# Kernel optimization log

Hardware: AMD Instinct MI355X
Metric: run time of the kernel (lower is better)

Reference implementation:

```python
import jax, jax.numpy as jnp
import numpy as np

# Per-task block sizes, sorted descending (powers of 2), as in _InverseLogDetCache
N = (262144, 65536, 16384)
TOTAL = 262144 + 65536 + 16384  # 344064
DIAG_SHIFT = 10.0  # keeps Schur complement S away from 0 (plays role of noise)


def setup_inputs() -> dict:
    key = jax.random.key(0)
    ks = jax.random.split(key, 14)
    rn = lambda k, n: jax.random.normal(k, (n,), dtype=jnp.float32)
    return {
        "lam00_re": rn(ks[0], N[0]) + DIAG_SHIFT,
        "lam00_im": rn(ks[1], N[0]),
        "lam01_re": rn(ks[2], N[0]),
        "lam01_im": rn(ks[3], N[0]),
        "lam02_re": rn(ks[4], N[0]),
        "lam02_im": rn(ks[5], N[0]),
        "lam11_re": rn(ks[6], N[1]) + DIAG_SHIFT,
        "lam11_im": rn(ks[7], N[1]),
        "lam12_re": rn(ks[8], N[1]),
        "lam12_im": rn(ks[9], N[1]),
        "lam22_re": rn(ks[10], N[2]) + DIAG_SHIFT,
        "lam22_im": rn(ks[11], N[2]),
        "z_re": rn(ks[12], TOTAL),
        "z_im": rn(ks[13], TOTAL),
    }


def _step(A, B, lam_ll, n_l):
    """One recursive block Schur-complement update.
    A: (Ra, Ra, na) complex current inverse; B: (Ra*r, n_l) off-diag lam block;
    lam_ll: (n_l,) diagonal lam; returns updated A (R+1, R+1, n_l) and logdet inc."""
    Ra, na = A.shape[0], A.shape[-1]
    r = na // n_l
    Bvec = B.reshape(Ra, -1)                              # (Ra, na)
    T = (Bvec[None, :, :] * A).sum(1).reshape(-1, n_l)    # (R, n_l), R = Ra*r
    M = (B.conj() * T).sum(0)                             # (n_l,)
    S = lam_ll - M                                        # Schur complement diag
    logdet_inc = jnp.log(jnp.abs(S)).sum()
    P = T / S                                             # (R, n_l)
    C = P[:, None, :] * T[None, :, :].conj()              # (R, R, n_l)
    # scatter-add old inverse A into the refined block structure of C
    ii0, ii1, ii2 = jnp.meshgrid(jnp.arange(Ra), jnp.arange(Ra), jnp.arange(na), indexing='ij')
    ii0, ii1, ii2 = ii0.ravel(), ii1.ravel(), ii2.ravel()
    jj0 = ii2 % n_l
    jj1 = ii2 // n_l
    C = C.at[ii0 * r + jj1, ii1 * r + jj1, jj0].add(A.reshape(-1))
    ur = jnp.concatenate([C, -P[:, None, :]], axis=1)                       # (R, R+1, n_l)
    br = jnp.concatenate([-P.conj()[None, :, :], (1.0 / S)[None, None, :]], axis=1)  # (1, R+1, n_l)
    return jnp.concatenate([ur, br], axis=0), logdet_inc


def _forward(lams, z):
    A = (1.0 / lams[(0, 0)])[None, None, :]               # (1, 1, N[0])
    logdet = jnp.log(jnp.abs(lams[(0, 0)])).sum()
    for l in range(1, len(N)):
        B = jnp.concatenate([lams[(k, l)] for k in range(l)], axis=0).reshape(-1, N[l])
        A, inc = _step(A, B, lams[(l, l)], N[l])
        logdet = logdet + inc
    # tilde-to-tilde gram matrix solve: z (TOTAL,) -> (1, R, n_min) * A, sum block rows
    n_min = N[-1]
    zb = z.reshape(1, -1, n_min)                          # (1, 21, n_min)
    zout = (zb * A).sum(-2).reshape(-1)                   # (TOTAL,)
    return A, logdet, zout


def reference(lam00_re, lam00_im, lam01_re, lam01_im, lam02_re, lam02_im,
              lam11_re, lam11_im, lam12_re, lam12_im, lam22_re, lam22_im,
              z_re, z_im):
    lams = {
        (0, 0): lam00_re + 1j * lam00_im,
        (0, 1): lam01_re + 1j * lam01_im,
        (0, 2): lam02_re + 1j * lam02_im,
        (1, 1): lam11_re + 1j * lam11_im,
        (1, 2): lam12_re + 1j * lam12_im,
        (2, 2): lam22_re + 1j * lam22_im,
    }
    z = z_re + 1j * z_im
    A, logdet, zout = _forward(lams, z)
    return (jnp.stack([A.real, A.imag]), logdet, jnp.stack([zout.real, zout.imag]))
```

## Files before the change

kernel.cpp:

```cpp
#include <hip/hip_runtime.h>

#define N2 16384
#define N1 65536

#define OUT_AIM 7225344
#define OUT_LD  14450688
#define OUT_ZRE 14450689
#define OUT_ZIM 14794753

#define L_T2R  0
#define L_T2I  1280
#define L_M2   2560
#define L_SC   3072
#define L_IS2R 9728
#define L_IS2I 9792
#define L_RED  9856
#define L_TOT  9864

#define SC(idx, u, jl) lds[L_SC + (((idx)*4 + (u)) * 64) + (jl)]

#define NTST2(addr, v0, v1) do {                                   \
    union { float f[2]; long L; } _u; _u.f[0] = (v0); _u.f[1] = (v1); \
    __builtin_nontemporal_store(_u.L, (long*)(addr)); } while (0)

__global__ __launch_bounds__(448) void fused_kernel(
    const float* __restrict__ l00r, const float* __restrict__ l00i,
    const float* __restrict__ l01r, const float* __restrict__ l01i,
    const float* __restrict__ l02r, const float* __restrict__ l02i,
    const float* __restrict__ l11r, const float* __restrict__ l11i,
    const float* __restrict__ l12r, const float* __restrict__ l12i,
    const float* __restrict__ l22r, const float* __restrict__ l22i,
    const float* __restrict__ zre,  const float* __restrict__ zim,
    float* __restrict__ out, double* __restrict__ ld_partial)
{
    __shared__ float lds[L_TOT];
    const int t   = threadIdx.x;
    const int jl  = t & 63;
    const int j0  = blockIdx.x * 64;
    const bool y0 = (blockIdx.y == 0);
    float ld = 0.f;

    if (t < 256) {
        const int u = t >> 6;
        const int m = u * N2 + (j0 + jl);

        float i0r[4], i0i[4], t1r[4], t1i[4], p1r[4], p1i[4];
        float m1r = 0.f, m1i = 0.f;
#pragma unroll
        for (int k = 0; k < 4; ++k) {
            const int i = k * N1 + m;
            const float ar = l00r[i], ai = l00i[i];
            const float br = l01r[i], bi = l01i[i];
            const float d  = ar*ar + ai*ai;
            const float rd = 1.f / d;
            if (y0) ld += 0.5f * logf(d);
            const float xr = ar * rd, xi = -ai * rd;
            i0r[k] = xr; i0i[k] = xi;
            const float tr = br*xr - bi*xi;
            const float ti = br*xi + bi*xr;
            t1r[k] = tr; t1i[k] = ti;
            m1r += br*tr + bi*ti;
            m1i += br*ti - bi*tr;
        }
        const float s1r = l11r[m] - m1r;
        const float s1i = l11i[m] - m1i;
        const float ds1 = s1r*s1r + s1i*s1i;
        if (y0) ld += 0.5f * logf(ds1);
        const float rds1 = 1.f / ds1;
        const float is1r = s1r * rds1, is1i = -s1i * rds1;
#pragma unroll
        for (int k = 0; k < 4; ++k) {
            p1r[k] = t1r[k]*is1r - t1i[k]*is1i;
            p1i[k] = t1r[k]*is1i + t1i[k]*is1r;
        }

        float bcr[5], bci[5];
#pragma unroll
        for (int a = 0; a < 4; ++a) { bcr[a] = l02r[a*N1+m]; bci[a] = l02i[a*N1+m]; }
        bcr[4] = l12r[m]; bci[4] = l12i[m];

        float wr = -bcr[4], wi = -bci[4];
#pragma unroll
        for (int b = 0; b < 4; ++b) {
            wr += bcr[b]*t1r[b] + bci[b]*t1i[b];
            wi += bci[b]*t1r[b] - bcr[b]*t1i[b];
        }
        float ur[5], ui[5];
#pragma unroll
        for (int a = 0; a < 4; ++a) {
            ur[a] = p1r[a]*wr - p1i[a]*wi + bcr[a]*i0r[a] - bci[a]*i0i[a];
            ui[a] = p1r[a]*wi + p1i[a]*wr + bcr[a]*i0i[a] + bci[a]*i0r[a];
        }
        {
            float vr = bcr[4]*is1r - bci[4]*is1i;
            float vi = bcr[4]*is1i + bci[4]*is1r;
#pragma unroll
            for (int b = 0; b < 4; ++b) {
                vr -= bcr[b]*p1r[b] + bci[b]*p1i[b];
                vi -= bci[b]*p1r[b] - bcr[b]*p1i[b];
            }
            ur[4] = vr; ui[4] = vi;
        }
        float m2r = 0.f, m2i = 0.f;
#pragma unroll
        for (int a = 0; a < 5; ++a) {
            lds[L_T2R + (a*4+u)*64 + jl] = ur[a];
            lds[L_T2I + (a*4+u)*64 + jl] = ui[a];
            m2r += bcr[a]*ur[a] + bci[a]*ui[a];
            m2i += bcr[a]*ui[a] - bci[a]*ur[a];
        }
        lds[L_M2 + (0*4+u)*64 + jl] = m2r;
        lds[L_M2 + (1*4+u)*64 + jl] = m2i;
#pragma unroll
        for (int b = 0; b < 4; ++b) {
            SC(b,      u, jl) = t1r[b];  SC(4+b,  u, jl) = t1i[b];
            SC(8+b,    u, jl) = p1r[b];  SC(12+b, u, jl) = p1i[b];
            SC(16+b,   u, jl) = i0r[b];  SC(20+b, u, jl) = i0i[b];
        }
        SC(24, u, jl) = is1r;  SC(25, u, jl) = is1i;
    }
    __syncthreads();

    if (t < 64) {
        float s2r = l22r[j0 + t], s2i = l22i[j0 + t];
#pragma unroll
        for (int u = 0; u < 4; ++u) {
            s2r -= lds[L_M2 + (0*4+u)*64 + t];
            s2i -= lds[L_M2 + (1*4+u)*64 + t];
        }
        const float ds2  = s2r*s2r + s2i*s2i;
        const float rds2 = 1.f / ds2;
        lds[L_IS2R + t] =  s2r * rds2;
        lds[L_IS2I + t] = -s2i * rds2;
        if (y0) ld += 0.5f * logf(ds2);
    }
    __syncthreads();

    const int g  = t >> 6;
    const int p  = blockIdx.y * 7 + g;
    const int l  = t & 63;
    const int h  = l >> 5;
    const int c  = l & 31;
    const int c2 = 2*c;
    const int j2 = j0 + c2;

    const float is2r0 = lds[L_IS2R + c2],   is2r1 = lds[L_IS2R + c2+1];
    const float is2i0 = lds[L_IS2I + c2],   is2i1 = lds[L_IS2I + c2+1];

    float zar0=0.f, zai0=0.f, zar1=0.f, zai1=0.f;

    if (p == 20) {
#pragma unroll
        for (int qi = 0; qi < 11; ++qi) {
            const int q = 2*qi + h;
            if (q >= 21) continue;
            float ar0, ai0, ar1, ai1;
            if (q < 20) {
                const float tr0 = lds[L_T2R + q*64 + c2], tr1 = lds[L_T2R + q*64 + c2+1];
                const float ti0 = lds[L_T2I + q*64 + c2], ti1 = lds[L_T2I + q*64 + c2+1];
                ar0 = -(tr0*is2r0 - ti0*is2i0);  ai0 = tr0*is2i0 + ti0*is2r0;
                ar1 = -(tr1*is2r1 - ti1*is2i1);  ai1 = tr1*is2i1 + ti1*is2r1;
            } else { ar0=is2r0; ai0=is2i0; ar1=is2r1; ai1=is2i1; }
            NTST2(out + (p*21+q)*N2 + j2,           ar0, ar1);
            NTST2(out + OUT_AIM + (p*21+q)*N2 + j2, ai0, ai1);
            const float zr0 = zre[q*N2+j2], zr1 = zre[q*N2+j2+1];
            const float zi0 = zim[q*N2+j2], zi1 = zim[q*N2+j2+1];
            zar0 += zr0*ar0 - zi0*ai0;  zai0 += zr0*ai0 + zi0*ar0;
            zar1 += zr1*ar1 - zi1*ai1;  zai1 += zr1*ai1 + zi1*ar1;
        }
    } else {
        const int a_p = p >> 2, u_p = p & 3;
        const float tpr0 = lds[L_T2R + p*64 + c2], tpr1 = lds[L_T2R + p*64 + c2+1];
        const float tpi0 = lds[L_T2I + p*64 + c2], tpi1 = lds[L_T2I + p*64 + c2+1];
        const float ppr0 = tpr0*is2r0 - tpi0*is2i0, ppi0 = tpr0*is2i0 + tpi0*is2r0;
        const float ppr1 = tpr1*is2r1 - tpi1*is2i1, ppi1 = tpr1*is2i1 + tpi1*is2r1;
        float par0=0.f, pai0=0.f, par1=0.f, pai1=0.f;
        if (a_p < 4) {
            par0 = SC(8+a_p,  u_p, c2);   pai0 = SC(12+a_p, u_p, c2);
            par1 = SC(8+a_p,  u_p, c2+1); pai1 = SC(12+a_p, u_p, c2+1);
        }
#pragma unroll
        for (int qi = 0; qi < 11; ++qi) {
            const int q = 2*qi + h;
            if (q >= 21) continue;
            float ar0, ai0, ar1, ai1;
            if (q < 20) {
                const float tr0 = lds[L_T2R + q*64 + c2], tr1 = lds[L_T2R + q*64 + c2+1];
                const float ti0 = lds[L_T2I + q*64 + c2], ti1 = lds[L_T2I + q*64 + c2+1];
                ar0 = ppr0*tr0 + ppi0*ti0;  ai0 = ppi0*tr0 - ppr0*ti0;
                ar1 = ppr1*tr1 + ppi1*ti1;  ai1 = ppi1*tr1 - ppr1*ti1;
                if ((q & 3) == u_p) {
                    const int b = q >> 2;
                    if (a_p < 4) {
                        if (b < 4) {
                            const float tbr0 = SC(b, u_p, c2),   tbi0 = SC(4+b, u_p, c2);
                            const float tbr1 = SC(b, u_p, c2+1), tbi1 = SC(4+b, u_p, c2+1);
                            ar0 += par0*tbr0 + pai0*tbi0;  ai0 += pai0*tbr0 - par0*tbi0;
                            ar1 += par1*tbr1 + pai1*tbi1;  ai1 += pai1*tbr1 - par1*tbi1;
                            if (b == a_p) {
                                ar0 += SC(16+a_p, u_p, c2);   ai0 += SC(20+a_p, u_p, c2);
                                ar1 += SC(16+a_p, u_p, c2+1); ai1 += SC(20+a_p, u_p, c2+1);
                            }
                        } else { ar0 -= par0; ai0 -= pai0; ar1 -= par1; ai1 -= pai1; }
                    } else {
                        if (b < 4) {
                            ar0 -= SC(8+b, u_p, c2);   ai0 += SC(12+b, u_p, c2);
                            ar1 -= SC(8+b, u_p, c2+1); ai1 += SC(12+b, u_p, c2+1);
                        } else {
                            ar0 += SC(24, u_p, c2);   ai0 += SC(25, u_p, c2);
                            ar1 += SC(24, u_p, c2+1); ai1 += SC(25, u_p, c2+1);
                        }
                    }
                }
            } else { ar0 = -ppr0; ai0 = -ppi0; ar1 = -ppr1; ai1 = -ppi1; }
            NTST2(out + (p*21+q)*N2 + j2,           ar0, ar1);
            NTST2(out + OUT_AIM + (p*21+q)*N2 + j2, ai0, ai1);
            const float zr0 = zre[q*N2+j2], zr1 = zre[q*N2+j2+1];
            const float zi0 = zim[q*N2+j2], zi1 = zim[q*N2+j2+1];
            zar0 += zr0*ar0 - zi0*ai0;  zai0 += zr0*ai0 + zi0*ar0;
            zar1 += zr1*ar1 - zi1*ai1;  zai1 += zr1*ai1 + zi1*ar1;
        }
    }

    zar0 += __shfl_xor(zar0, 32, 64);  zai0 += __shfl_xor(zai0, 32, 64);
    zar1 += __shfl_xor(zar1, 32, 64);  zai1 += __shfl_xor(zai1, 32, 64);
    {
        const int src = l >> 1;
        const float e_r = __shfl(zar0, src, 64), o_r = __shfl(zar1, src, 64);
        const float e_i = __shfl(zai0, src, 64), o_i = __shfl(zai1, src, 64);
        const float zvr = (l & 1) ? o_r : e_r;
        const float zvi = (l & 1) ? o_i : e_i;
        __builtin_nontemporal_store(zvr, out + OUT_ZRE + p*N2 + j0 + l);
        __builtin_nontemporal_store(zvi, out + OUT_ZIM + p*N2 + j0 + l);
    }

    if (y0) {
        float v = ld;
#pragma unroll
        for (int off = 32; off > 0; off >>= 1) v += __shfl_down(v, off, 64);
        __syncthreads();
        if (jl == 0) lds[L_RED + g] = v;
        __syncthreads();
        if (t == 0) {
            double s = 0.0;
#pragma unroll
            for (int w = 0; w < 7; ++w) s += (double)lds[L_RED + w];
            ld_partial[blockIdx.x] = s;
        }
    }
}

__global__ void finalize_kernel(const double* __restrict__ part,
                                float* __restrict__ out) {
    double v = part[threadIdx.x];
#pragma unroll
    for (int off = 32; off > 0; off >>= 1) v += __shfl_down(v, off, 64);
    __shared__ double wsum[4];
    if ((threadIdx.x & 63) == 0) wsum[threadIdx.x >> 6] = v;
    __syncthreads();
    if (threadIdx.x == 0)
        out[OUT_LD] = (float)(wsum[0] + wsum[1] + wsum[2] + wsum[3]);
}

extern "C" void kernel_launch(void* const* d_in, const int* in_sizes, int n_in,
                              void* d_out, int out_size, void* d_ws, size_t ws_size,
                              hipStream_t stream)
{
    const float* l00r = (const float*)d_in[0];
    const float* l00i = (const float*)d_in[1];
    const float* l01r = (const float*)d_in[2];
    const float* l01i = (const float*)d_in[3];
    const float* l02r = (const float*)d_in[4];
    const float* l02i = (const float*)d_in[5];
    const float* l11r = (const float*)d_in[6];
    const float* l11i = (const float*)d_in[7];
    const float* l12r = (const float*)d_in[8];
    const float* l12i = (const float*)d_in[9];
    const float* l22r = (const float*)d_in[10];
    const float* l22i = (const float*)d_in[11];
    const float* zre  = (const float*)d_in[12];
    const float* zim  = (const float*)d_in[13];
    float*  out        = (float*)d_out;
    double* ld_partial = (double*)d_ws;

    fused_kernel<<<dim3(N2/64, 3), dim3(448), 0, stream>>>(
        l00r,l00i,l01r,l01i,l02r,l02i,l11r,l11i,l12r,l12i,l22r,l22i,
        zre,zim, out, ld_partial);
    finalize_kernel<<<1, 256, 0, stream>>>(ld_partial, out);
}
```

Before: 113.7 us.

## Split fused kernel into Schur pass and wide write pass through workspace

```diff
diff --git a/kernel.cpp b/kernel.cpp
--- a/kernel.cpp
+++ b/kernel.cpp
@@ -8,42 +8,34 @@
 #define OUT_ZRE 14450689
 #define OUT_ZIM 14794753
 
-#define L_T2R  0
-#define L_T2I  1280
-#define L_M2   2560
-#define L_SC   3072
-#define L_IS2R 9728
-#define L_IS2I 9792
-#define L_RED  9856
-#define L_TOT  9864
-
-#define SC(idx, u, jl) lds[L_SC + (((idx)*4 + (u)) * 64) + (jl)]
-
-#define NTST2(addr, v0, v1) do {                                   \
-    union { float f[2]; long L; } _u; _u.f[0] = (v0); _u.f[1] = (v1); \
-    __builtin_nontemporal_store(_u.L, (long*)(addr)); } while (0)
-
-__global__ __launch_bounds__(448) void fused_kernel(
+#define WS_T2R  0
+#define WS_T2I  (20*N2)
+#define WS_IS2R (40*N2)
+#define WS_IS2I (41*N2)
+#define WS_SC   (42*N2)
+#define WS_FLOATS (146*N2)
+
+__global__ __launch_bounds__(256) void schur_kernel(
     const float* __restrict__ l00r, const float* __restrict__ l00i,
     const float* __restrict__ l01r, const float* __restrict__ l01i,
     const float* __restrict__ l02r, const float* __restrict__ l02i,
     const float* __restrict__ l11r, const float* __restrict__ l11i,
     const float* __restrict__ l12r, const float* __restrict__ l12i,
     const float* __restrict__ l22r, const float* __restrict__ l22i,
-    const float* __restrict__ zre,  const float* __restrict__ zim,
-    float* __restrict__ out, double* __restrict__ ld_partial)
+    float* __restrict__ ws, double* __restrict__ ld_partial)
 {
-    __shared__ float lds[L_TOT];
-    const int t   = threadIdx.x;
-    const int jl  = t & 63;
-    const int j0  = blockIdx.x * 64;
-    const bool y0 = (blockIdx.y == 0);
+    __shared__ float lds[520];
+    const int t  = threadIdx.x;
+    const int u  = t >> 6;
+    const int jl = t & 63;
+    const int j0 = blockIdx.x * 64;
+    const int j  = j0 + jl;
+    const int m  = u * N2 + j;
     float ld = 0.f;
 
-    if (t < 256) {
-        const int u = t >> 6;
-        const int m = u * N2 + (j0 + jl);
-
+#define SCW(idx) ws[WS_SC + ((idx)*4 + u)*N2 + j]
+
+    {
         float i0r[4], i0i[4], t1r[4], t1i[4], p1r[4], p1i[4];
         float m1r = 0.f, m1i = 0.f;
 #pragma unroll
@@ -53,7 +45,7 @@
             const float br = l01r[i], bi = l01i[i];
             const float d  = ar*ar + ai*ai;
             const float rd = 1.f / d;
-            if (y0) ld += 0.5f * logf(d);
+            ld += 0.5f * logf(d);
             const float xr = ar * rd, xi = -ai * rd;
             i0r[k] = xr; i0i[k] = xi;
             const float tr = br*xr - bi*xi;
@@ -65,7 +57,7 @@
         const float s1r = l11r[m] - m1r;
         const float s1i = l11i[m] - m1i;
         const float ds1 = s1r*s1r + s1i*s1i;
-        if (y0) ld += 0.5f * logf(ds1);
+        ld += 0.5f * logf(ds1);
         const float rds1 = 1.f / ds1;
         const float is1r = s1r * rds1, is1i = -s1i * rds1;
 #pragma unroll
@@ -104,162 +96,161 @@
         float m2r = 0.f, m2i = 0.f;
 #pragma unroll
         for (int a = 0; a < 5; ++a) {
-            lds[L_T2R + (a*4+u)*64 + jl] = ur[a];
-            lds[L_T2I + (a*4+u)*64 + jl] = ui[a];
+            ws[WS_T2R + (a*4+u)*N2 + j] = ur[a];
+            ws[WS_T2I + (a*4+u)*N2 + j] = ui[a];
             m2r += bcr[a]*ur[a] + bci[a]*ui[a];
             m2i += bcr[a]*ui[a] - bci[a]*ur[a];
         }
-        lds[L_M2 + (0*4+u)*64 + jl] = m2r;
-        lds[L_M2 + (1*4+u)*64 + jl] = m2i;
+        lds[(0*4+u)*64 + jl] = m2r;
+        lds[(1*4+u)*64 + jl] = m2i;
 #pragma unroll
         for (int b = 0; b < 4; ++b) {
-            SC(b,      u, jl) = t1r[b];  SC(4+b,  u, jl) = t1i[b];
-            SC(8+b,    u, jl) = p1r[b];  SC(12+b, u, jl) = p1i[b];
-            SC(16+b,   u, jl) = i0r[b];  SC(20+b, u, jl) = i0i[b];
-        }
-        SC(24, u, jl) = is1r;  SC(25, u, jl) = is1i;
+            SCW(b)      = t1r[b];  SCW(4+b)  = t1i[b];
+            SCW(8+b)    = p1r[b];  SCW(12+b) = p1i[b];
+            SCW(16+b)   = i0r[b];  SCW(20+b) = i0i[b];
+        }
+        SCW(24) = is1r;  SCW(25) = is1i;
     }
     __syncthreads();
 
     if (t < 64) {
         float s2r = l22r[j0 + t], s2i = l22i[j0 + t];
 #pragma unroll
-        for (int u = 0; u < 4; ++u) {
-            s2r -= lds[L_M2 + (0*4+u)*64 + t];
-            s2i -= lds[L_M2 + (1*4+u)*64 + t];
+        for (int uu = 0; uu < 4; ++uu) {
+            s2r -= lds[(0*4+uu)*64 + t];
+            s2i -= lds[(1*4+uu)*64 + t];
         }
         const float ds2  = s2r*s2r + s2i*s2i;
         const float rds2 = 1.f / ds2;
-        lds[L_IS2R + t] =  s2r * rds2;
-        lds[L_IS2I + t] = -s2i * rds2;
-        if (y0) ld += 0.5f * logf(ds2);
-    }
-    __syncthreads();
-
-    const int g  = t >> 6;
-    const int p  = blockIdx.y * 7 + g;
-    const int l  = t & 63;
-    const int h  = l >> 5;
-    const int c  = l & 31;
-    const int c2 = 2*c;
-    const int j2 = j0 + c2;
-
-    const float is2r0 = lds[L_IS2R + c2],   is2r1 = lds[L_IS2R + c2+1];
-    const float is2i0 = lds[L_IS2I + c2],   is2i1 = lds[L_IS2I + c2+1];
-
-    float zar0=0.f, zai0=0.f, zar1=0.f, zai1=0.f;
-
-    if (p == 20) {
-#pragma unroll
-        for (int qi = 0; qi < 11; ++qi) {
-            const int q = 2*qi + h;
-            if (q >= 21) continue;
-            float ar0, ai0, ar1, ai1;
-            if (q < 20) {
-                const float tr0 = lds[L_T2R + q*64 + c2], tr1 = lds[L_T2R + q*64 + c2+1];
-                const float ti0 = lds[L_T2I + q*64 + c2], ti1 = lds[L_T2I + q*64 + c2+1];
-                ar0 = -(tr0*is2r0 - ti0*is2i0);  ai0 = tr0*is2i0 + ti0*is2r0;
-                ar1 = -(tr1*is2r1 - ti1*is2i1);  ai1 = tr1*is2i1 + ti1*is2r1;
-            } else { ar0=is2r0; ai0=is2i0; ar1=is2r1; ai1=is2i1; }
-            NTST2(out + (p*21+q)*N2 + j2,           ar0, ar1);
-            NTST2(out + OUT_AIM + (p*21+q)*N2 + j2, ai0, ai1);
-            const float zr0 = zre[q*N2+j2], zr1 = zre[q*N2+j2+1];
-            const float zi0 = zim[q*N2+j2], zi1 = zim[q*N2+j2+1];
-            zar0 += zr0*ar0 - zi0*ai0;  zai0 += zr0*ai0 + zi0*ar0;
-            zar1 += zr1*ar1 - zi1*ai1;  zai1 += zr1*ai1 + zi1*ar1;
-        }
-    } else {
-        const int a_p = p >> 2, u_p = p & 3;
-        const float tpr0 = lds[L_T2R + p*64 + c2], tpr1 = lds[L_T2R + p*64 + c2+1];
-        const float tpi0 = lds[L_T2I + p*64 + c2], tpi1 = lds[L_T2I + p*64 + c2+1];
-        const float ppr0 = tpr0*is2r0 - tpi0*is2i0, ppi0 = tpr0*is2i0 + tpi0*is2r0;
-        const float ppr1 = tpr1*is2r1 - tpi1*is2i1, ppi1 = tpr1*is2i1 + tpi1*is2r1;
-        float par0=0.f, pai0=0.f, par1=0.f, pai1=0.f;
-        if (a_p < 4) {
-            par0 = SC(8+a_p,  u_p, c2);   pai0 = SC(12+a_p, u_p, c2);
-            par1 = SC(8+a_p,  u_p, c2+1); pai1 = SC(12+a_p, u_p, c2+1);
-        }
-#pragma unroll
-        for (int qi = 0; qi < 11; ++qi) {
-            const int q = 2*qi + h;
-            if (q >= 21) continue;
-            float ar0, ai0, ar1, ai1;
-            if (q < 20) {
-                const float tr0 = lds[L_T2R + q*64 + c2], tr1 = lds[L_T2R + q*64 + c2+1];
-                const float ti0 = lds[L_T2I + q*64 + c2], ti1 = lds[L_T2I + q*64 + c2+1];
-                ar0 = ppr0*tr0 + ppi0*ti0;  ai0 = ppi0*tr0 - ppr0*ti0;
-                ar1 = ppr1*tr1 + ppi1*ti1;  ai1 = ppi1*tr1 - ppr1*ti1;
-                if ((q & 3) == u_p) {
-                    const int b = q >> 2;
-                    if (a_p < 4) {
-                        if (b < 4) {
-                            const float tbr0 = SC(b, u_p, c2),   tbi0 = SC(4+b, u_p, c2);
-                            const float tbr1 = SC(b, u_p, c2+1), tbi1 = SC(4+b, u_p, c2+1);
-                            ar0 += par0*tbr0 + pai0*tbi0;  ai0 += pai0*tbr0 - par0*tbi0;
-                            ar1 += par1*tbr1 + pai1*tbi1;  ai1 += pai1*tbr1 - par1*tbi1;
-                            if (b == a_p) {
-                                ar0 += SC(16+a_p, u_p, c2);   ai0 += SC(20+a_p, u_p, c2);
-                                ar1 += SC(16+a_p, u_p, c2+1); ai1 += SC(20+a_p, u_p, c2+1);
-                            }
-                        } else { ar0 -= par0; ai0 -= pai0; ar1 -= par1; ai1 -= pai1; }
-                    } else {
-                        if (b < 4) {
-                            ar0 -= SC(8+b, u_p, c2);   ai0 += SC(12+b, u_p, c2);
-                            ar1 -= SC(8+b, u_p, c2+1); ai1 += SC(12+b, u_p, c2+1);
-                        } else {
-                            ar0 += SC(24, u_p, c2);   ai0 += SC(25, u_p, c2);
-                            ar1 += SC(24, u_p, c2+1); ai1 += SC(25, u_p, c2+1);
-                        }
-                    }
-                }
-            } else { ar0 = -ppr0; ai0 = -ppi0; ar1 = -ppr1; ai1 = -ppi1; }
-            NTST2(out + (p*21+q)*N2 + j2,           ar0, ar1);
-            NTST2(out + OUT_AIM + (p*21+q)*N2 + j2, ai0, ai1);
-            const float zr0 = zre[q*N2+j2], zr1 = zre[q*N2+j2+1];
-            const float zi0 = zim[q*N2+j2], zi1 = zim[q*N2+j2+1];
-            zar0 += zr0*ar0 - zi0*ai0;  zai0 += zr0*ai0 + zi0*ar0;
-            zar1 += zr1*ar1 - zi1*ai1;  zai1 += zr1*ai1 + zi1*ar1;
-        }
-    }
-
-    zar0 += __shfl_xor(zar0, 32, 64);  zai0 += __shfl_xor(zai0, 32, 64);
-    zar1 += __shfl_xor(zar1, 32, 64);  zai1 += __shfl_xor(zai1, 32, 64);
+        ws[WS_IS2R + j0 + t] =  s2r * rds2;
+        ws[WS_IS2I + j0 + t] = -s2i * rds2;
+        ld += 0.5f * logf(ds2);
+    }
+
     {
-        const int src = l >> 1;
-        const float e_r = __shfl(zar0, src, 64), o_r = __shfl(zar1, src, 64);
-        const float e_i = __shfl(zai0, src, 64), o_i = __shfl(zai1, src, 64);
-        const float zvr = (l & 1) ? o_r : e_r;
-        const float zvi = (l & 1) ? o_i : e_i;
-        __builtin_nontemporal_store(zvr, out + OUT_ZRE + p*N2 + j0 + l);
-        __builtin_nontemporal_store(zvi, out + OUT_ZIM + p*N2 + j0 + l);
-    }
-
-    if (y0) {
         float v = ld;
 #pragma unroll
         for (int off = 32; off > 0; off >>= 1) v += __shfl_down(v, off, 64);
         __syncthreads();
-        if (jl == 0) lds[L_RED + g] = v;
+        if (jl == 0) lds[512 + (t >> 6)] = v;
         __syncthreads();
         if (t == 0) {
             double s = 0.0;
 #pragma unroll
-            for (int w = 0; w < 7; ++w) s += (double)lds[L_RED + w];
+            for (int w = 0; w < 4; ++w) s += (double)lds[512 + w];
             ld_partial[blockIdx.x] = s;
         }
     }
+#undef SCW
 }
 
-__global__ void finalize_kernel(const double* __restrict__ part,
-                                float* __restrict__ out) {
-    double v = part[threadIdx.x];
-#pragma unroll
-    for (int off = 32; off > 0; off >>= 1) v += __shfl_down(v, off, 64);
-    __shared__ double wsum[4];
-    if ((threadIdx.x & 63) == 0) wsum[threadIdx.x >> 6] = v;
-    __syncthreads();
-    if (threadIdx.x == 0)
-        out[OUT_LD] = (float)(wsum[0] + wsum[1] + wsum[2] + wsum[3]);
+__global__ __launch_bounds__(256) void write_kernel(
+    const float* __restrict__ zre, const float* __restrict__ zim,
+    const float* __restrict__ ws, const double* __restrict__ ld_partial,
+    float* __restrict__ out)
+{
+    const int p = blockIdx.y;
+    const int j = blockIdx.x * 512 + threadIdx.x * 2;
+
+#define WF2(off)      (*reinterpret_cast<const float2*>(ws + (off) + j))
+#define SCF2(idx,uu)  (*reinterpret_cast<const float2*>(ws + WS_SC + ((idx)*4 + (uu))*N2 + j))
+#define OST2(off, a, b) do { float2 _o; _o.x=(a); _o.y=(b);                   \
+    *reinterpret_cast<float2*>(out + (off) + j) = _o; } while (0)
+
+    const float2 i2r = WF2(WS_IS2R);
+    const float2 i2i = WF2(WS_IS2I);
+
+    const bool is20 = (p == 20);
+    const int  ap = p >> 2, up = p & 3;
+    float pr0=0.f, pi0=0.f, pr1=0.f, pi1=0.f;
+    float2 par = {0.f, 0.f}, pai = {0.f, 0.f};
+    if (!is20) {
+        const float2 t2r = WF2(WS_T2R + p*N2);
+        const float2 t2i = WF2(WS_T2I + p*N2);
+        pr0 = t2r.x*i2r.x - t2i.x*i2i.x;  pi0 = t2r.x*i2i.x + t2i.x*i2r.x;
+        pr1 = t2r.y*i2r.y - t2i.y*i2i.y;  pi1 = t2r.y*i2i.y + t2i.y*i2r.y;
+        if (ap < 4) { par = SCF2(8+ap, up);  pai = SCF2(12+ap, up); }
+    }
+
+    float zar0=0.f, zai0=0.f, zar1=0.f, zai1=0.f;
+
+#pragma unroll
+    for (int q = 0; q < 20; ++q) {
+        const float2 tq = WF2(WS_T2R + q*N2);
+        const float2 uq = WF2(WS_T2I + q*N2);
+        const float2 zr = *reinterpret_cast<const float2*>(zre + q*N2 + j);
+        const float2 zi = *reinterpret_cast<const float2*>(zim + q*N2 + j);
+        float ar0, ai0, ar1, ai1;
+        if (is20) {
+            ar0 = -(tq.x*i2r.x - uq.x*i2i.x);  ai0 = tq.x*i2i.x + uq.x*i2r.x;
+            ar1 = -(tq.y*i2r.y - uq.y*i2i.y);  ai1 = tq.y*i2i.y + uq.y*i2r.y;
+        } else {
+            ar0 = pr0*tq.x + pi0*uq.x;  ai0 = pi0*tq.x - pr0*uq.x;
+            ar1 = pr1*tq.y + pi1*uq.y;  ai1 = pi1*tq.y - pr1*uq.y;
+            if ((q & 3) == up) {
+                const int b = q >> 2;
+                if (ap < 4) {
+                    if (b < 4) {
+                        const float2 tb = SCF2(b,   up);
+                        const float2 ub = SCF2(4+b, up);
+                        ar0 += par.x*tb.x + pai.x*ub.x;  ai0 += pai.x*tb.x - par.x*ub.x;
+                        ar1 += par.y*tb.y + pai.y*ub.y;  ai1 += pai.y*tb.y - par.y*ub.y;
+                        if (b == ap) {
+                            const float2 dr = SCF2(16+ap, up);
+                            const float2 di = SCF2(20+ap, up);
+                            ar0 += dr.x; ai0 += di.x; ar1 += dr.y; ai1 += di.y;
+                        }
+                    } else {
+                        ar0 -= par.x; ai0 -= pai.x; ar1 -= par.y; ai1 -= pai.y;
+                    }
+                } else {
+                    if (b < 4) {
+                        const float2 qr = SCF2(8+b,  up);
+                        const float2 qi = SCF2(12+b, up);
+                        ar0 -= qr.x; ai0 += qi.x; ar1 -= qr.y; ai1 += qi.y;
+                    } else {
+                        const float2 sr = SCF2(24, up);
+                        const float2 si = SCF2(25, up);
+                        ar0 += sr.x; ai0 += si.x; ar1 += sr.y; ai1 += si.y;
+                    }
+                }
+            }
+        }
+        OST2((p*21+q)*N2,           ar0, ar1);
+        OST2(OUT_AIM + (p*21+q)*N2, ai0, ai1);
+        zar0 += zr.x*ar0 - zi.x*ai0;  zai0 += zr.x*ai0 + zi.x*ar0;
+        zar1 += zr.y*ar1 - zi.y*ai1;  zai1 += zr.y*ai1 + zi.y*ar1;
+    }
+    {
+        const float2 zr = *reinterpret_cast<const float2*>(zre + 20*N2 + j);
+        const float2 zi = *reinterpret_cast<const float2*>(zim + 20*N2 + j);
+        float ar0, ai0, ar1, ai1;
+        if (is20) { ar0 = i2r.x; ai0 = i2i.x; ar1 = i2r.y; ai1 = i2i.y; }
+        else      { ar0 = -pr0;  ai0 = -pi0;  ar1 = -pr1;  ai1 = -pi1; }
+        OST2((p*21+20)*N2,           ar0, ar1);
+        OST2(OUT_AIM + (p*21+20)*N2, ai0, ai1);
+        zar0 += zr.x*ar0 - zi.x*ai0;  zai0 += zr.x*ai0 + zi.x*ar0;
+        zar1 += zr.y*ar1 - zi.y*ai1;  zai1 += zr.y*ai1 + zi.y*ar1;
+    }
+
+    out[OUT_ZRE + p*N2 + j]     = zar0;
+    out[OUT_ZRE + p*N2 + j + 1] = zar1;
+    out[OUT_ZIM + p*N2 + j]     = zai0;
+    out[OUT_ZIM + p*N2 + j + 1] = zai1;
+
+    if (blockIdx.x == 0 && p == 0) {
+        __shared__ double wsum[4];
+        double v = ld_partial[threadIdx.x];
+#pragma unroll
+        for (int off = 32; off > 0; off >>= 1) v += __shfl_down(v, off, 64);
+        if ((threadIdx.x & 63) == 0) wsum[threadIdx.x >> 6] = v;
+        __syncthreads();
+        if (threadIdx.x == 0)
+            out[OUT_LD] = (float)(wsum[0] + wsum[1] + wsum[2] + wsum[3]);
+    }
+#undef WF2
+#undef SCF2
+#undef OST2
 }
 
 extern "C" void kernel_launch(void* const* d_in, const int* in_sizes, int n_in,
@@ -280,11 +271,13 @@
     const float* l22i = (const float*)d_in[11];
     const float* zre  = (const float*)d_in[12];
     const float* zim  = (const float*)d_in[13];
-    float*  out        = (float*)d_out;
-    double* ld_partial = (double*)d_ws;
-
-    fused_kernel<<<dim3(N2/64, 3), dim3(448), 0, stream>>>(
+    float*  out = (float*)d_out;
+    float*  wsf = (float*)d_ws;
+    double* ldp = (double*)(wsf + WS_FLOATS);
+
+    schur_kernel<<<dim3(N2/64), dim3(256), 0, stream>>>(
         l00r,l00i,l01r,l01i,l02r,l02i,l11r,l11i,l12r,l12i,l22r,l22i,
-        zre,zim, out, ld_partial);
-    finalize_kernel<<<1, 256, 0, stream>>>(ld_partial, out);
+        wsf, ldp);
+    write_kernel<<<dim3(32, 21), dim3(256), 0, stream>>>(
+        zre, zim, wsf, ldp, out);
 }
```

New measurement: 121.8 us. +7.1%, slower.
